# Kernel optimization log

Measured on AMD Instinct MI355X. Metric: run time of the kernel, lower is better.

## Reference

```python
import jax, jax.numpy as jnp
import numpy as np

NUM_CLASSES = 2
LOG2_NC = float(np.log2(NUM_CLASSES))


def _conv(x, w, b=None):
    # NCHW conv, stride 1, SAME padding (kernel 3 pad 1 or kernel 1 pad 0)
    y = jax.lax.conv_general_dilated(x, w, (1, 1), 'SAME',
                                     dimension_numbers=('NCHW', 'OIHW', 'NCHW'))
    if b is not None:
        y = y + b[None, :, None, None]
    return y


def _uncertainty_map(ds):
    # entropy over class dim, thresholded to {0,1}
    logp = jax.nn.log_softmax(ds, axis=1)            # [B,C,H,W]
    prob = jnp.exp(logp)
    # torch uses log2(prob + 1e-6); replicate exactly
    ent = -jnp.sum(prob * jnp.log2(prob + 1e-6), axis=1) / LOG2_NC  # [B,H,W]
    return (ent >= 0.001).astype(jnp.float32)


def _unob(tar, amap):
    # vectorized UnoB with S=3: interior pixels with tar!=0 get pro=0 unless
    # 4*tar == sum of the 4-neighborhood (i.e. locally constant label)
    t = tar  # [B,H,W] int
    nb = t[:, 2:, 1:-1] + t[:, :-2, 1:-1] + t[:, 1:-1, 2:] + t[:, 1:-1, :-2]
    center = t[:, 1:-1, 1:-1]
    inner_pro = jnp.where((center != 0) & (4 * center != nb), 0.0, 1.0)
    pro = jnp.ones_like(amap)
    pro = pro.at[:, 1:-1, 1:-1].set(inner_pro)
    return amap * pro


def setup_inputs() -> dict:
    key = jax.random.key(0)
    ks = jax.random.split(key, 6)
    B, C, H, W = 8, 128, 128, 128
    return {
        'x': jax.random.normal(ks[0], (B, C, H, W), jnp.float32),
        'skip': jax.random.normal(ks[1], (B, C, H, W), jnp.float32),
        'tar': jax.random.randint(ks[2], (B, 1, H, W), 0, NUM_CLASSES, jnp.int64)
            if jax.config.jax_enable_x64 else
            jax.random.randint(ks[2], (B, 1, H, W), 0, NUM_CLASSES).astype(jnp.int32),
        'W1': jax.random.normal(ks[3], (128, 256, 3, 3), jnp.float32) * 0.05,
        'b1': jnp.zeros((128,), jnp.float32),
        'W2': jax.random.normal(ks[4], (128, 128, 3, 3), jnp.float32) * 0.05,
        'b2': jnp.zeros((128,), jnp.float32),
        'Wds': jax.random.normal(ks[5], (NUM_CLASSES, 128, 1, 1), jnp.float32) * 0.05,
    }


def reference(x, skip, tar, W1, b1, W2, b2, Wds):
    h = jnp.concatenate([x, skip], axis=1)            # [B,2*dim,H,W]
    h = jax.nn.leaky_relu(_conv(h, W1, b1), 0.01)     # [B,dim,H,W]
    h = jax.nn.leaky_relu(_conv(h, W2, b2), 0.01)
    ds = _conv(h, Wds)                                # [B,num_classes,H,W]
    amap = _uncertainty_map(ds)                       # [B,H,W]
    amap = _unob(tar[:, 0], amap)                     # UnoB refinement, S=3
    return h, ds, amap
```

## Files before the change

### kernel.cpp

```cpp
#include <hip/hip_runtime.h>

typedef float f32x16 __attribute__((ext_vector_type(16)));
typedef short bf16x8 __attribute__((ext_vector_type(8)));
typedef unsigned int u32;

static __device__ __forceinline__ unsigned short f2bf(float f) {
  union { float f; unsigned int u; } v;
  v.f = f;
  return (unsigned short)((v.u + 0x7FFFu + ((v.u >> 16) & 1u)) >> 16);
}

static __device__ __forceinline__ void gl_lds16(const unsigned short* g,
                                                unsigned short* l) {
  __builtin_amdgcn_global_load_lds(
      (const __attribute__((address_space(1))) u32*)g,
      (__attribute__((address_space(3))) u32*)l, 16, 0, 0);
}

#define VMCNT0 asm volatile("s_waitcnt vmcnt(0)" ::: "memory")
#define LGKM0 asm volatile("s_waitcnt lgkmcnt(0)" ::: "memory")
#define BAR __builtin_amdgcn_s_barrier()
#define SCHEDB __builtin_amdgcn_sched_barrier(0)
#define PRIO1 __builtin_amdgcn_s_setprio(1)
#define PRIO0 __builtin_amdgcn_s_setprio(0)

__global__ __launch_bounds__(256) void convert_weights(
    const float* __restrict__ W1, const float* __restrict__ W2,
    unsigned short* __restrict__ W1b, unsigned short* __restrict__ W2b,
    unsigned short* __restrict__ zp) {
  if (blockIdx.x == 1728) {
    uint4* z = (uint4*)zp;
    z[threadIdx.x] = make_uint4(0, 0, 0, 0);
    z[256 + threadIdx.x] = make_uint4(0, 0, 0, 0);
    return;
  }
  int i = blockIdx.x * 256 + threadIdx.x;
  if (i < 294912) {
    int e = i & 7, co = (i >> 3) & 127, r = i >> 10;
    int tap = r % 9, pc = r / 9;
    int ci = (pc >> 1) * 16 + (pc & 1) * 8 + e;
    W1b[i] = f2bf(W1[(co * 256 + ci) * 9 + tap]);
  } else {
    int j = i - 294912;
    if (j < 147456) {
      int e = j & 7, co = (j >> 3) & 127, r = j >> 10;
      int tap = r % 9, pc = r / 9;
      int ci = (pc >> 1) * 16 + (pc & 1) * 8 + e;
      W2b[j] = f2bf(W2[(co * 128 + ci) * 9 + tap]);
    }
  }
}

__global__ __launch_bounds__(256) void transpose_to_bf16(
    const float* __restrict__ x, const float* __restrict__ skip,
    unsigned short* __restrict__ dst) {
  int bid = blockIdx.x;
  const float* src = (bid < 1024) ? x : skip;
  int cigb = (bid < 1024) ? 0 : 16;
  int row = bid & 1023;
  int b = row >> 7, y = row & 127;
  const float* s = src + (long)b * 128 * 16384 + (long)y * 128;
  for (int it = 0; it < 8; ++it) {
    int u = it * 256 + (int)threadIdx.x;
    int cig = u >> 7, px = u & 127;
    unsigned short pk[8];
#pragma unroll
    for (int e = 0; e < 8; ++e)
      pk[e] = f2bf(s[(long)(cig * 8 + e) * 16384 + px]);
    uint4 vv;
    vv.x = (unsigned)pk[0] | ((unsigned)pk[1] << 16);
    vv.y = (unsigned)pk[2] | ((unsigned)pk[3] << 16);
    vv.z = (unsigned)pk[4] | ((unsigned)pk[5] << 16);
    vv.w = (unsigned)pk[6] | ((unsigned)pk[7] << 16);
    *(uint4*)(&dst[(((long)row * 32 + cigb + cig) * 130 + px + 1) * 8]) = vv;
  }
  if (cigb == 0 && threadIdx.x < 64) {
    int g = threadIdx.x >> 1;
    long col = (threadIdx.x & 1) * 129L;
    *(uint4*)(&dst[(((long)row * 32 + g) * 130 + col) * 8]) = make_uint4(0, 0, 0, 0);
  }
}

template <int CIN, bool FUSE_DS>
__global__ __launch_bounds__(512, 2) void conv3x3(
    const unsigned short* __restrict__ src,
    const unsigned short* __restrict__ wt,
    const float* __restrict__ bias,
    const unsigned short* __restrict__ zp,
    unsigned short* __restrict__ dst_bf16,
    float* __restrict__ dst_f32,
    const float* __restrict__ wds,
    const int* __restrict__ tar,
    float* __restrict__ ds,
    float* __restrict__ amap) {
  constexpr int CPG = CIN / 8;
  constexpr int NC = CIN / 16;
  __shared__ unsigned short in_tile[2][1664 * 8];
  __shared__ unsigned short wt_tile[2][2304 * 8];
  __shared__ unsigned short scr[64 * 8];
  __shared__ float sb[128];
  __shared__ float w0s[128], w1s[128];
  __shared__ float sc[4 * 4 * 2 * 32];

  const int tid = threadIdx.x;
  const int wg = (blockIdx.x & 7) * 32 + (blockIdx.x >> 3);
  const int b = wg >> 5;
  const int y0 = (wg & 31) * 4;
  const int lane = tid & 63, wave = tid >> 6;
  const int wco = wave & 1, wrow = wave >> 1;
  const int l31 = lane & 31, kh = lane >> 5;

  if (tid < 128) {
    sb[tid] = bias[tid];
    if constexpr (FUSE_DS) {
      w0s[tid] = wds[tid];
      w1s[tid] = wds[128 + tid];
    }
  }

  const unsigned short* gb[8];
  unsigned short* ld0[8];
  int gst[8];
  int lst[8];
#pragma unroll
  for (int i = 0; i < 8; ++i) {
    const int o = wave * 8 + i;
    if (o < 36) {
      gb[i] = wt + o * 512 + lane * 8;
      gst[i] = 18432;
      ld0[i] = &wt_tile[0][(size_t)o * 512];
      lst[i] = 18432;
    } else if (o < 62) {
      const int q = o - 36;
      const int p = q / 13, j = q - p * 13;
      const int s = j * 64 + lane;
      const int hy = s / 130, hx = s - hy * 130;
      const int gy = y0 - 1 + hy;
      const bool ok = (s < 780) && (gy >= 0) && (gy < 128);
      gb[i] = ok ? src + ((size_t)((b * 128 + gy) * CPG) + p) * 1040 + hx * 8
                 : zp + lane * 8;
      gst[i] = ok ? 2080 : 0;
      ld0[i] = &in_tile[0][(size_t)(p * 832 + j * 64) * 8];
      lst[i] = 1664 * 8;
    } else {
      gb[i] = zp + lane * 8;
      gst[i] = 0;
      ld0[i] = &scr[0];
      lst[i] = 0;
    }
  }

  f32x16 acc[2][4] = {};

#pragma unroll
  for (int i = 0; i < 8; ++i) gl_lds16(gb[i], ld0[i]);
  VMCNT0;
  LGKM0;
  BAR;
  SCHEDB;

  for (int cic = 0; cic < NC; ++cic) {
    const int cur = cic & 1;
    const int nbuf = cur ^ 1;
    const bool more = (cic + 1 < NC);

    const unsigned short* it = &in_tile[cur][0];
    const unsigned short* wl = &wt_tile[cur][0];
    const size_t ib = (size_t)kh * (832 * 8);
    const size_t wb = (size_t)kh * 9216;

    bf16x8 xa0, xa1, xb0, xb1, xb2, xb3;
    bf16x8 ya0, ya1, yb0, yb1, yb2, yb3;

#define LD_TAP(T, A0, A1, B0, B1, B2, B3)                                      \
  {                                                                            \
    constexpr int ky_ = (T) / 3, kx_ = (T) % 3;                                \
    const int hy_ = ky_ + wrow;                                                \
    A0 = *(const bf16x8*)(&wl[wb + (size_t)((T)*128 + wco * 64 + l31) * 8]);   \
    A1 = *(const bf16x8*)(&wl[wb + (size_t)((T)*128 + wco * 64 + 32 + l31) * 8]); \
    B0 = *(const bf16x8*)(&it[ib + (size_t)(hy_ * 130 + l31 + kx_) * 8]);      \
    B1 = *(const bf16x8*)(&it[ib + (size_t)(hy_ * 130 + 32 + l31 + kx_) * 8]); \
    B2 = *(const bf16x8*)(&it[ib + (size_t)(hy_ * 130 + 64 + l31 + kx_) * 8]); \
    B3 = *(const bf16x8*)(&it[ib + (size_t)(hy_ * 130 + 96 + l31 + kx_) * 8]); \
  }

#define MFMA_TAP(A0, A1, B0, B1, B2, B3)                                       \
  {                                                                            \
    acc[0][0] = __builtin_amdgcn_mfma_f32_32x32x16_bf16(A0, B0, acc[0][0], 0, 0, 0); \
    acc[0][1] = __builtin_amdgcn_mfma_f32_32x32x16_bf16(A0, B1, acc[0][1], 0, 0, 0); \
    acc[0][2] = __builtin_amdgcn_mfma_f32_32x32x16_bf16(A0, B2, acc[0][2], 0, 0, 0); \
    acc[0][3] = __builtin_amdgcn_mfma_f32_32x32x16_bf16(A0, B3, acc[0][3], 0, 0, 0); \
    acc[1][0] = __builtin_amdgcn_mfma_f32_32x32x16_bf16(A1, B0, acc[1][0], 0, 0, 0); \
    acc[1][1] = __builtin_amdgcn_mfma_f32_32x32x16_bf16(A1, B1, acc[1][1], 0, 0, 0); \
    acc[1][2] = __builtin_amdgcn_mfma_f32_32x32x16_bf16(A1, B2, acc[1][2], 0, 0, 0); \
    acc[1][3] = __builtin_amdgcn_mfma_f32_32x32x16_bf16(A1, B3, acc[1][3], 0, 0, 0); \
  }

    LD_TAP(0, xa0, xa1, xb0, xb1, xb2, xb3);
    LD_TAP(1, ya0, ya1, yb0, yb1, yb2, yb3);
    SCHEDB;

    if (more) {
#pragma unroll
      for (int i = 0; i < 4; ++i)
        gl_lds16(gb[i] + (size_t)(cic + 1) * gst[i],
                 ld0[i] + (size_t)nbuf * lst[i]);
    }
    SCHEDB;
    BAR;
    PRIO1;
    MFMA_TAP(xa0, xa1, xb0, xb1, xb2, xb3);
    LD_TAP(2, xa0, xa1, xb0, xb1, xb2, xb3);
    SCHEDB;
    MFMA_TAP(ya0, ya1, yb0, yb1, yb2, yb3);
    LD_TAP(3, ya0, ya1, yb0, yb1, yb2, yb3);
    SCHEDB;
    MFMA_TAP(xa0, xa1, xb0, xb1, xb2, xb3);
    LD_TAP(4, xa0, xa1, xb0, xb1, xb2, xb3);
    SCHEDB;
    PRIO0;

    if (more) {
#pragma unroll
      for (int i = 4; i < 8; ++i)
        gl_lds16(gb[i] + (size_t)(cic + 1) * gst[i],
                 ld0[i] + (size_t)nbuf * lst[i]);
    }
    SCHEDB;
    BAR;
    PRIO1;
    MFMA_TAP(ya0, ya1, yb0, yb1, yb2, yb3);
    LD_TAP(5, ya0, ya1, yb0, yb1, yb2, yb3);
    SCHEDB;
    MFMA_TAP(xa0, xa1, xb0, xb1, xb2, xb3);
    LD_TAP(6, xa0, xa1, xb0, xb1, xb2, xb3);
    SCHEDB;
    MFMA_TAP(ya0, ya1, yb0, yb1, yb2, yb3);
    LD_TAP(7, ya0, ya1, yb0, yb1, yb2, yb3);
    SCHEDB;
    PRIO0;

    BAR;
    PRIO1;
    MFMA_TAP(xa0, xa1, xb0, xb1, xb2, xb3);
    LD_TAP(8, xa0, xa1, xb0, xb1, xb2, xb3);
    SCHEDB;
    MFMA_TAP(ya0, ya1, yb0, yb1, yb2, yb3);
    SCHEDB;
    MFMA_TAP(xa0, xa1, xb0, xb1, xb2, xb3);
    PRIO0;
#undef LD_TAP
#undef MFMA_TAP

    SCHEDB;
    LGKM0;
    VMCNT0;
    BAR;
    SCHEDB;
  }

  const int gyo = y0 + wrow;
  float pd[4][2] = {};
#pragma unroll
  for (int fc = 0; fc < 2; ++fc) {
#pragma unroll
    for (int fp = 0; fp < 4; ++fp) {
      const int px = fp * 32 + l31;
      if constexpr (!FUSE_DS) {
#pragma unroll
        for (int rg = 0; rg < 4; ++rg) {
          const int co0 = wco * 64 + fc * 32 + rg * 8 + kh * 4;
          unsigned short pk[4];
#pragma unroll
          for (int q = 0; q < 4; ++q) {
            float v = acc[fc][fp][rg * 4 + q] + sb[co0 + q];
            v = v > 0.f ? v : 0.01f * v;
            pk[q] = f2bf(v);
          }
          uint2 o;
          o.x = (unsigned)pk[0] | ((unsigned)pk[1] << 16);
          o.y = (unsigned)pk[2] | ((unsigned)pk[3] << 16);
          *(uint2*)(&dst_bf16[(((long)(b * 128 + gyo) * 16 + (co0 >> 3)) * 130 + px + 1) * 8 +
                              kh * 4]) = o;
        }
      } else {
#pragma unroll
        for (int rg = 0; rg < 4; ++rg) {
          const int co0 = wco * 64 + fc * 32 + rg * 8 + kh * 4;
          float4 wv0 = *(const float4*)(&w0s[co0]);
          float4 wv1 = *(const float4*)(&w1s[co0]);
#pragma unroll
          for (int q = 0; q < 4; ++q) {
            float v = acc[fc][fp][rg * 4 + q] + sb[co0 + q];
            v = v > 0.f ? v : 0.01f * v;
            dst_f32[((long)(b * 128 + co0 + q) << 14) + (gyo << 7) + px] = v;
            float wq0 = (q == 0) ? wv0.x : (q == 1) ? wv0.y : (q == 2) ? wv0.z : wv0.w;
            float wq1 = (q == 0) ? wv1.x : (q == 1) ? wv1.y : (q == 2) ? wv1.z : wv1.w;
            pd[fp][0] += wq0 * v;
            pd[fp][1] += wq1 * v;
          }
        }
      }
    }
  }

  if constexpr (!FUSE_DS) {
    if (tid < 128) {
      int row = tid >> 5, g = (tid >> 1) & 15;
      long col = (tid & 1) * 129L;
      *(uint4*)(&dst_bf16[(((long)(b * 128 + y0 + row) * 16 + g) * 130 + col) * 8]) =
          make_uint4(0, 0, 0, 0);
    }
  } else {
#pragma unroll
    for (int fp = 0; fp < 4; ++fp)
#pragma unroll
      for (int c = 0; c < 2; ++c)
        pd[fp][c] += __shfl_xor(pd[fp][c], 32, 64);
    if (wco == 1 && kh == 0) {
#pragma unroll
      for (int fp = 0; fp < 4; ++fp)
#pragma unroll
        for (int c = 0; c < 2; ++c)
          sc[((wrow * 4 + fp) * 2 + c) * 32 + l31] = pd[fp][c];
    }
    __syncthreads();
    if (wco == 0 && kh == 0) {
      const int* tb = tar + (long)b * 16384;
#pragma unroll
      for (int fp = 0; fp < 4; ++fp) {
        const int px = fp * 32 + l31;
        float a0 = pd[fp][0] + sc[((wrow * 4 + fp) * 2 + 0) * 32 + l31];
        float a1 = pd[fp][1] + sc[((wrow * 4 + fp) * 2 + 1) * 32 + l31];
        ds[((long)b * 2) * 16384 + (gyo << 7) + px] = a0;
        ds[((long)b * 2 + 1) * 16384 + (gyo << 7) + px] = a1;
        float m = fmaxf(a0, a1);
        float e0 = expf(a0 - m), e1 = expf(a1 - m);
        float s = e0 + e1;
        float p0f = e0 / s, p1f = e1 / s;
        float ent = -(p0f * log2f(p0f + 1e-6f) + p1f * log2f(p1f + 1e-6f));
        float un = ent >= 0.001f ? 1.f : 0.f;
        float pro = 1.f;
        if (gyo > 0 && gyo < 127 && px > 0 && px < 127) {
          int c = tb[(gyo << 7) + px];
          if (c != 0) {
            int nb2 = tb[((gyo - 1) << 7) + px] + tb[((gyo + 1) << 7) + px] +
                      tb[(gyo << 7) + px - 1] + tb[(gyo << 7) + px + 1];
            if (4 * c != nb2) pro = 0.f;
          }
        }
        amap[((long)(b * 128 + gyo) << 7) + px] = un * pro;
      }
    }
  }
}

extern "C" void kernel_launch(void* const* d_in, const int* in_sizes, int n_in,
                              void* d_out, int out_size, void* d_ws, size_t ws_size,
                              hipStream_t stream) {
  const float* x    = (const float*)d_in[0];
  const float* skip = (const float*)d_in[1];
  const int*   tar  = (const int*)d_in[2];
  const float* W1   = (const float*)d_in[3];
  const float* b1   = (const float*)d_in[4];
  const float* W2   = (const float*)d_in[5];
  const float* b2   = (const float*)d_in[6];
  const float* Wds  = (const float*)d_in[7];

  float* out_h  = (float*)d_out;
  float* out_ds = out_h + 16777216;
  float* out_am = out_ds + 262144;

  unsigned short* W1b = (unsigned short*)d_ws;
  unsigned short* W2b = W1b + 294912;
  unsigned short* zp  = W2b + 147456;
  unsigned short* h1  = (unsigned short*)((char*)d_ws + (1u << 20));

  unsigned short* h0 = (unsigned short*)d_out;

  convert_weights<<<1729, 256, 0, stream>>>(W1, W2, W1b, W2b, zp);
  transpose_to_bf16<<<2048, 256, 0, stream>>>(x, skip, h0);
  conv3x3<256, false><<<256, 512, 0, stream>>>(h0, W1b, b1, zp, h1, nullptr,
                                               nullptr, nullptr, nullptr, nullptr);
  conv3x3<128, true><<<256, 512, 0, stream>>>(h1, W2b, b2, zp, nullptr, out_h,
                                              Wds, tar, out_ds, out_am);
}
```

Before: 147.3 us.

## Merge weight conversion and input transpose kernels, reshape conv prefetch and priority

The weight-conversion and input-transpose kernels become a single prep launch that splits its block range between the two jobs, which removes one kernel launch and its gap. In the conv main loop, all eight next-chunk global-to-LDS prefetches are now issued together before the first barrier instead of being split across two barriers. The wave priority raise and drop now wrap each MFMA group instead of each larger region. Issuing all prefetches at once may put more pressure on the memory pipeline, and the finer priority toggles add a few extra instructions.

Measured after the change: 142.8 us. 3.0% less time.

```diff
diff --git a/kernel.cpp b/kernel.cpp
--- a/kernel.cpp
+++ b/kernel.cpp
@@ -24,41 +24,41 @@
 #define PRIO1 __builtin_amdgcn_s_setprio(1)
 #define PRIO0 __builtin_amdgcn_s_setprio(0)
 
-__global__ __launch_bounds__(256) void convert_weights(
+__global__ __launch_bounds__(256) void prep(
+    const float* __restrict__ x, const float* __restrict__ skip,
     const float* __restrict__ W1, const float* __restrict__ W2,
-    unsigned short* __restrict__ W1b, unsigned short* __restrict__ W2b,
-    unsigned short* __restrict__ zp) {
-  if (blockIdx.x == 1728) {
-    uint4* z = (uint4*)zp;
-    z[threadIdx.x] = make_uint4(0, 0, 0, 0);
-    z[256 + threadIdx.x] = make_uint4(0, 0, 0, 0);
-    return;
-  }
-  int i = blockIdx.x * 256 + threadIdx.x;
-  if (i < 294912) {
-    int e = i & 7, co = (i >> 3) & 127, r = i >> 10;
-    int tap = r % 9, pc = r / 9;
-    int ci = (pc >> 1) * 16 + (pc & 1) * 8 + e;
-    W1b[i] = f2bf(W1[(co * 256 + ci) * 9 + tap]);
-  } else {
-    int j = i - 294912;
-    if (j < 147456) {
-      int e = j & 7, co = (j >> 3) & 127, r = j >> 10;
+    unsigned short* __restrict__ dst, unsigned short* __restrict__ W1b,
+    unsigned short* __restrict__ W2b, unsigned short* __restrict__ zp) {
+  const int bid = blockIdx.x;
+  if (bid >= 2048) {
+    const int cb = bid - 2048;
+    if (cb == 1728) {
+      uint4* z = (uint4*)zp;
+      z[threadIdx.x] = make_uint4(0, 0, 0, 0);
+      z[256 + threadIdx.x] = make_uint4(0, 0, 0, 0);
+      return;
+    }
+    int i = cb * 256 + (int)threadIdx.x;
+    if (i < 294912) {
+      int e = i & 7, co = (i >> 3) & 127, r = i >> 10;
       int tap = r % 9, pc = r / 9;
       int ci = (pc >> 1) * 16 + (pc & 1) * 8 + e;
-      W2b[j] = f2bf(W2[(co * 128 + ci) * 9 + tap]);
-    }
-  }
-}
-
-__global__ __launch_bounds__(256) void transpose_to_bf16(
-    const float* __restrict__ x, const float* __restrict__ skip,
-    unsigned short* __restrict__ dst) {
-  int bid = blockIdx.x;
+      W1b[i] = f2bf(W1[(co * 256 + ci) * 9 + tap]);
+    } else {
+      int j = i - 294912;
+      if (j < 147456) {
+        int e = j & 7, co = (j >> 3) & 127, r = j >> 10;
+        int tap = r % 9, pc = r / 9;
+        int ci = (pc >> 1) * 16 + (pc & 1) * 8 + e;
+        W2b[j] = f2bf(W2[(co * 128 + ci) * 9 + tap]);
+      }
+    }
+    return;
+  }
   const float* src = (bid < 1024) ? x : skip;
-  int cigb = (bid < 1024) ? 0 : 16;
-  int row = bid & 1023;
-  int b = row >> 7, y = row & 127;
+  const int cigb = (bid < 1024) ? 0 : 16;
+  const int row = bid & 1023;
+  const int b = row >> 7, y = row & 127;
   const float* s = src + (long)b * 128 * 16384 + (long)y * 128;
   for (int it = 0; it < 8; ++it) {
     int u = it * 256 + (int)threadIdx.x;
@@ -186,6 +186,7 @@
 
 #define MFMA_TAP(A0, A1, B0, B1, B2, B3)                                       \
   {                                                                            \
+    PRIO1;                                                                     \
     acc[0][0] = __builtin_amdgcn_mfma_f32_32x32x16_bf16(A0, B0, acc[0][0], 0, 0, 0); \
     acc[0][1] = __builtin_amdgcn_mfma_f32_32x32x16_bf16(A0, B1, acc[0][1], 0, 0, 0); \
     acc[0][2] = __builtin_amdgcn_mfma_f32_32x32x16_bf16(A0, B2, acc[0][2], 0, 0, 0); \
@@ -194,6 +195,7 @@
     acc[1][1] = __builtin_amdgcn_mfma_f32_32x32x16_bf16(A1, B1, acc[1][1], 0, 0, 0); \
     acc[1][2] = __builtin_amdgcn_mfma_f32_32x32x16_bf16(A1, B2, acc[1][2], 0, 0, 0); \
     acc[1][3] = __builtin_amdgcn_mfma_f32_32x32x16_bf16(A1, B3, acc[1][3], 0, 0, 0); \
+    PRIO0;                                                                     \
   }
 
     LD_TAP(0, xa0, xa1, xb0, xb1, xb2, xb3);
@@ -202,13 +204,12 @@
 
     if (more) {
 #pragma unroll
-      for (int i = 0; i < 4; ++i)
+      for (int i = 0; i < 8; ++i)
         gl_lds16(gb[i] + (size_t)(cic + 1) * gst[i],
                  ld0[i] + (size_t)nbuf * lst[i]);
     }
     SCHEDB;
     BAR;
-    PRIO1;
     MFMA_TAP(xa0, xa1, xb0, xb1, xb2, xb3);
     LD_TAP(2, xa0, xa1, xb0, xb1, xb2, xb3);
     SCHEDB;
@@ -218,17 +219,8 @@
     MFMA_TAP(xa0, xa1, xb0, xb1, xb2, xb3);
     LD_TAP(4, xa0, xa1, xb0, xb1, xb2, xb3);
     SCHEDB;
-    PRIO0;
-
-    if (more) {
-#pragma unroll
-      for (int i = 4; i < 8; ++i)
-        gl_lds16(gb[i] + (size_t)(cic + 1) * gst[i],
-                 ld0[i] + (size_t)nbuf * lst[i]);
-    }
-    SCHEDB;
+
     BAR;
-    PRIO1;
     MFMA_TAP(ya0, ya1, yb0, yb1, yb2, yb3);
     LD_TAP(5, ya0, ya1, yb0, yb1, yb2, yb3);
     SCHEDB;
@@ -238,17 +230,14 @@
     MFMA_TAP(ya0, ya1, yb0, yb1, yb2, yb3);
     LD_TAP(7, ya0, ya1, yb0, yb1, yb2, yb3);
     SCHEDB;
-    PRIO0;
 
     BAR;
-    PRIO1;
     MFMA_TAP(xa0, xa1, xb0, xb1, xb2, xb3);
     LD_TAP(8, xa0, xa1, xb0, xb1, xb2, xb3);
     SCHEDB;
     MFMA_TAP(ya0, ya1, yb0, yb1, yb2, yb3);
     SCHEDB;
     MFMA_TAP(xa0, xa1, xb0, xb1, xb2, xb3);
-    PRIO0;
 #undef LD_TAP
 #undef MFMA_TAP
 
@@ -378,8 +367,7 @@
 
   unsigned short* h0 = (unsigned short*)d_out;
 
-  convert_weights<<<1729, 256, 0, stream>>>(W1, W2, W1b, W2b, zp);
-  transpose_to_bf16<<<2048, 256, 0, stream>>>(x, skip, h0);
+  prep<<<3777, 256, 0, stream>>>(x, skip, W1, W2, h0, W1b, W2b, zp);
   conv3x3<256, false><<<256, 512, 0, stream>>>(h0, W1b, b1, zp, h1, nullptr,
                                                nullptr, nullptr, nullptr, nullptr);
   conv3x3<128, true><<<256, 512, 0, stream>>>(h1, W2b, b2, zp, nullptr, out_h,
```
